# Kernel tuning notes

Measured on AMD Instinct MI355X. Metric: run time of the kernel, lower is better.

The kernel has to match this reference:

```python
import jax, jax.numpy as jnp
import numpy as np

IMAGE_SIZE = 800
OUT = 50          # feature map size
FEAT = 512
SCALES = (2.0, 4.0, 6.0)
RATIOS = (0.5, 1.0, 1.5)
A = len(SCALES) * len(RATIOS)          # 9 anchors per cell
POS_THR, NEG_THR = 0.7, 0.3
W_CONF, W_REG = 1.0, 5.0
SCALE = IMAGE_SIZE // OUT              # 16, stride of feature map


def _anchor_base():
    # order: ratio outer loop, scale inner loop (matches get_anchor_base)
    ws = jnp.array([s * r for r in RATIOS for s in SCALES], jnp.float32)  # [A]
    hs = jnp.array([s for r in RATIOS for s in SCALES], jnp.float32)      # [A]
    cx = (jnp.arange(OUT, dtype=jnp.float32) + 0.5)[:, None, None]        # grid dim0 -> x
    cy = (jnp.arange(OUT, dtype=jnp.float32) + 0.5)[None, :, None]        # grid dim1 -> y
    xmin = jnp.clip(cx - ws / 2, 0.0, OUT)
    xmax = jnp.clip(cx + ws / 2, 0.0, OUT)
    ymin = jnp.clip(cy - hs / 2, 0.0, OUT)
    ymax = jnp.clip(cy + hs / 2, 0.0, OUT)
    shp = (OUT, OUT, A)
    base = jnp.stack([jnp.broadcast_to(xmin, shp), jnp.broadcast_to(ymin, shp),
                      jnp.broadcast_to(xmax, shp), jnp.broadcast_to(ymax, shp)], axis=-1)
    return base.reshape(-1, 4)         # [N,4], N = OUT*OUT*A = 22500


def _iou(anchors, gt):
    # anchors [N,4], gt [B,M,4] (xyxy) -> iou [B,N,M]
    a = anchors[None, :, None, :]
    g = gt[:, None, :, :]
    ix1 = jnp.maximum(a[..., 0], g[..., 0]); iy1 = jnp.maximum(a[..., 1], g[..., 1])
    ix2 = jnp.minimum(a[..., 2], g[..., 2]); iy2 = jnp.minimum(a[..., 3], g[..., 3])
    inter = jnp.clip(ix2 - ix1, 0.0) * jnp.clip(iy2 - iy1, 0.0)
    area_a = (a[..., 2] - a[..., 0]) * (a[..., 3] - a[..., 1])
    area_g = (g[..., 2] - g[..., 0]) * (g[..., 3] - g[..., 1])
    return inter / (area_a + area_g - inter + 1e-8)


def _smooth_l1(d):
    ad = jnp.abs(d)
    return jnp.where(ad < 1.0, 0.5 * d * d, ad - 0.5)


def setup_inputs() -> dict:
    key = jax.random.key(0)
    ks = jax.random.split(key, 8)
    B, M = 16, 16
    features = jax.random.normal(ks[0], (B, FEAT, OUT, OUT), jnp.float32)
    # valid GT boxes in image coords: centers in [100,700], sizes in [32,200]
    cxy = jax.random.uniform(ks[1], (B, M, 2), jnp.float32, 100.0, 700.0)
    wh = jax.random.uniform(ks[2], (B, M, 2), jnp.float32, 32.0, 200.0)
    x1y1 = jnp.clip(cxy - wh / 2, 0.0, IMAGE_SIZE)
    x2y2 = jnp.clip(cxy + wh / 2, 0.0, IMAGE_SIZE)
    gt_boxes = jnp.concatenate([x1y1, x2y2], axis=-1)
    w1 = jax.random.normal(ks[3], (FEAT, FEAT, 3, 3), jnp.float32) * 0.02
    b1 = jnp.zeros((FEAT,), jnp.float32)
    w_cls = jax.random.normal(ks[4], (A, FEAT), jnp.float32) * 0.02
    b_cls = jnp.zeros((A,), jnp.float32)
    w_box = jax.random.normal(ks[5], (4 * A, FEAT), jnp.float32) * 0.02
    b_box = jnp.zeros((4 * A,), jnp.float32)
    return {"features": features, "gt_boxes": gt_boxes, "w1": w1, "b1": b1,
            "w_cls": w_cls, "b_cls": b_cls, "w_box": w_box, "b_box": b_box}


def reference(features, gt_boxes, w1, b1, w_cls, b_cls, w_box, b_box):
    B = features.shape[0]
    anchors = _anchor_base()                                   # [N,4]
    N = anchors.shape[0]

    # --- conv tower ---
    x = jax.lax.conv_general_dilated(features, w1, (1, 1), 'SAME') + b1[None, :, None, None]
    cls_map = jnp.einsum('bchw,ac->bahw', x, w_cls) + b_cls[None, :, None, None]   # [B,A,H,W]
    box_map = jnp.einsum('bchw,dc->bdhw', x, w_box) + b_box[None, :, None, None]   # [B,4A,H,W]
    logits = jnp.transpose(cls_map, (0, 2, 3, 1)).reshape(B, N)                    # [B,N]
    pred_off = jnp.transpose(box_map.reshape(B, A, 4, OUT, OUT), (0, 3, 4, 1, 2)).reshape(B, N, 4)

    # --- project gt to feature-map (anchor) coords, 'p2a' ---
    gt = gt_boxes / SCALE                                       # [B,M,4]

    # --- anchor/GT assignment ---
    iou = _iou(anchors, gt)                                     # [B,N,M]
    max_per_gt = jnp.max(iou, axis=1, keepdims=True)            # best anchor per gt
    pos_mask = ((iou == max_per_gt) & (max_per_gt > 0)) | (iou > POS_THR)  # [B,N,M]
    pos_mask = pos_mask.astype(jnp.float32)
    n_pos = jnp.maximum(pos_mask.sum(), 1.0)

    # --- gt offsets (standard tx,ty,tw,th) for every (anchor,gt) pair ---
    acx = (anchors[:, 0] + anchors[:, 2]) / 2
    acy = (anchors[:, 1] + anchors[:, 3]) / 2
    aw = jnp.maximum(anchors[:, 2] - anchors[:, 0], 1e-6)
    ah = jnp.maximum(anchors[:, 3] - anchors[:, 1], 1e-6)
    gcx = (gt[..., 0] + gt[..., 2]) / 2                         # [B,M]
    gcy = (gt[..., 1] + gt[..., 3]) / 2
    gw = jnp.maximum(gt[..., 2] - gt[..., 0], 1e-6)
    gh = jnp.maximum(gt[..., 3] - gt[..., 1], 1e-6)
    tx = (gcx[:, None, :] - acx[None, :, None]) / aw[None, :, None]   # [B,N,M]
    ty = (gcy[:, None, :] - acy[None, :, None]) / ah[None, :, None]
    tw = jnp.log(gw[:, None, :] / aw[None, :, None])
    th = jnp.log(gh[:, None, :] / ah[None, :, None])
    gt_off = jnp.stack([tx, ty, tw, th], axis=-1)               # [B,N,M,4]

    diff = gt_off - pred_off[:, :, None, :]
    reg_loss = (pos_mask[..., None] * _smooth_l1(diff)).sum() / (4.0 * n_pos)

    # --- classification loss: BCE-with-logits; positives=1, negatives=0 ---
    pos_loss = (pos_mask * jax.nn.softplus(-logits)[:, :, None]).sum() / n_pos
    neg_anchor = jnp.all(iou < NEG_THR, axis=2).astype(jnp.float32)   # [B,N]
    n_neg = jnp.maximum(neg_anchor.sum(), 1.0)
    neg_loss = (neg_anchor * jax.nn.softplus(logits)).sum() / n_neg
    cls_loss = 0.5 * (pos_loss + neg_loss)

    total_rpn_loss = W_CONF * cls_loss + W_REG * reg_loss

    # --- proposals from predicted offsets for all anchors ---
    pcx = acx[None, :] + pred_off[..., 0] * aw[None, :]
    pcy = acy[None, :] + pred_off[..., 1] * ah[None, :]
    pw = aw[None, :] * jnp.exp(pred_off[..., 2])
    ph = ah[None, :] * jnp.exp(pred_off[..., 3])
    proposals = jnp.stack([pcx - pw / 2, pcy - ph / 2, pcx + pw / 2, pcy + ph / 2], axis=-1)  # [B,N,4]

    return total_rpn_loss, proposals
```

## Files before the change

### kernel.cpp

```cpp
#include <hip/hip_runtime.h>
#include <hip/hip_bf16.h>
#include <stdint.h>


using bf16x8 = __attribute__((ext_vector_type(8))) __bf16;
using f32x4  = __attribute__((ext_vector_type(4))) float;

#define FT_CHUNK_STRIDE 2768896
#define W2_CHUNK_B 34560

__device__ __forceinline__ unsigned short f2bf(float f) {
  union { float f; unsigned u; } x; x.f = f;
  unsigned r = x.u + 0x7fffu + ((x.u >> 16) & 1u);
  return (unsigned short)(r >> 16);
}

__device__ __forceinline__ void gl_lds16(const void* g, void* l) {
  __builtin_amdgcn_global_load_lds(
      (const __attribute__((address_space(1))) void*)g,
      (__attribute__((address_space(3))) void*)l, 16, 0, 0);
}

__device__ __forceinline__ float sl1(float d) {
  float ad = fabsf(d);
  return ad < 1.f ? 0.5f * d * d : ad - 0.5f;
}
__device__ __forceinline__ float softplus_f(float x) {
  return fmaxf(x, 0.f) + log1pf(expf(-fabsf(x)));
}

__device__ __forceinline__ void anchor_strict(int n, float& ax1, float& ay1,
                                              float& ax2, float& ay2) {
  int ii = n / 450;
  int rem = n - ii * 450;
  int jj = rem / 9;
  int a  = rem - jj * 9;
  const float SC[3] = {2.f, 4.f, 6.f};
  const float RA[3] = {0.5f, 1.f, 1.5f};
  float w = __fmul_rn(SC[a % 3], RA[a / 3]);
  float h = SC[a % 3];
  float cx = __fadd_rn((float)ii, 0.5f);
  float cy = __fadd_rn((float)jj, 0.5f);
  float wh = __fmul_rn(w, 0.5f), hh = __fmul_rn(h, 0.5f);
  ax1 = fminf(fmaxf(__fsub_rn(cx, wh), 0.f), 50.f);
  ax2 = fminf(fmaxf(__fadd_rn(cx, wh), 0.f), 50.f);
  ay1 = fminf(fmaxf(__fsub_rn(cy, hh), 0.f), 50.f);
  ay2 = fminf(fmaxf(__fadd_rn(cy, hh), 0.f), 50.f);
}
__device__ __forceinline__ float iou_strict(float ax1, float ay1, float ax2, float ay2,
                                            float aarea, const float* __restrict__ g) {
  float gx1 = __fmul_rn(g[0], 0.0625f), gy1 = __fmul_rn(g[1], 0.0625f);
  float gx2 = __fmul_rn(g[2], 0.0625f), gy2 = __fmul_rn(g[3], 0.0625f);
  float ix1 = fmaxf(ax1, gx1), iy1 = fmaxf(ay1, gy1);
  float ix2 = fminf(ax2, gx2), iy2 = fminf(ay2, gy2);
  float inter = __fmul_rn(fmaxf(__fsub_rn(ix2, ix1), 0.f),
                          fmaxf(__fsub_rn(iy2, iy1), 0.f));
  float garea = __fmul_rn(__fsub_rn(gx2, gx1), __fsub_rn(gy2, gy1));
  float denom = __fadd_rn(__fsub_rn(__fadd_rn(aarea, garea), inter), 1e-8f);
  return __fdiv_rn(inter, denom);
}

__global__ __launch_bounds__(256) void k_featT(const float* __restrict__ feat,
                                               char* __restrict__ featT2) {
  const int tile = blockIdx.x;
  const int g    = blockIdx.y;
  const int b    = blockIdx.z;
  const int tid  = threadIdx.x;
  if (tile == 20) {
    uint4 z = {0, 0, 0, 0};
    for (int u = tid; u < 204 * 4; u += 256) {
      int p = u & 255; if (p >= 204) p -= 204;
      int c4 = u / 204;
      int ip, jp;
      if (p < 52)       { ip = 0;       jp = p; }
      else if (p < 104) { ip = 51;      jp = p - 52; }
      else if (p < 154) { ip = p - 103; jp = 0; }
      else              { ip = p - 153; jp = 51; }
      char* dst = featT2 + (size_t)(g * 4 + c4) * FT_CHUNK_STRIDE
                + (size_t)(b * 2704 + ip * 52 + jp) * 64;
      *(uint4*)(dst)      = z;
      *(uint4*)(dst + 16) = z;
      *(uint4*)(dst + 32) = z;
      *(uint4*)(dst + 48) = z;
    }
    return;
  }
  __shared__ __align__(16) unsigned short sT[128 * 132];
  const int pos0 = tile * 128;
  const float* fb = feat + (size_t)b * 1280000 + (size_t)(g * 128) * 2500;
  const int pq = tid & 31;
  const int rg = tid >> 5;
  const int p  = pos0 + pq * 4;
#pragma unroll
  for (int it = 0; it < 4; ++it) {
    int cb = it * 32 + rg * 4;
    float vv[4][4];
#pragma unroll
    for (int q = 0; q < 4; ++q) {
      const float* src = fb + (size_t)(cb + q) * 2500 + p;
      if (p + 3 < 2500) {
        float4 v = *(const float4*)src;
        vv[q][0] = v.x; vv[q][1] = v.y; vv[q][2] = v.z; vv[q][3] = v.w;
      } else {
#pragma unroll
        for (int e = 0; e < 4; ++e)
          vv[q][e] = fb[(size_t)(cb + q) * 2500 + min(p + e, 2499)];
      }
    }
#pragma unroll
    for (int pp = 0; pp < 4; ++pp) {
      ushort4 pk;
      pk.x = f2bf(vv[0][pp]); pk.y = f2bf(vv[1][pp]);
      pk.z = f2bf(vv[2][pp]); pk.w = f2bf(vv[3][pp]);
      *(ushort4*)&sT[(pq * 4 + pp) * 132 + cb] = pk;
    }
  }
  __syncthreads();
#pragma unroll
  for (int q2 = 0; q2 < 2; ++q2) {
    int u = tid + q2 * 256;
    int ch = u >> 7, pr = u & 127;
    int gp = pos0 + pr;
    if (gp >= 2500) continue;
    int i = gp / 50, j = gp - i * 50;
    char* dst = featT2 + (size_t)(g * 4 + ch) * FT_CHUNK_STRIDE
              + (size_t)(b * 2704 + (i + 1) * 52 + (j + 1)) * 64;
    const uint4* src = (const uint4*)&sT[pr * 132 + ch * 32];
    uint4 a0 = src[0], a1 = src[1], a2 = src[2], a3 = src[3];
    *(uint4*)(dst)      = a0;
    *(uint4*)(dst + 16) = a1;
    *(uint4*)(dst + 32) = a2;
    *(uint4*)(dst + 48) = a3;
  }
}

__global__ __launch_bounds__(128) void k_weff1(const float* __restrict__ w1,
                                               const float* __restrict__ wc,
                                               const float* __restrict__ wb,
                                               float* __restrict__ part,
                                               unsigned* __restrict__ zbuf) {
  const int t = threadIdx.x;
  if (blockIdx.x == 0 && blockIdx.y == 0) {
    for (int idx = t; idx < 264; idx += 128) zbuf[idx] = 0u;
  }
  __shared__ float sW[48][64];
  const int kmem = blockIdx.x * 128 + t;
  const int cz = blockIdx.y;
#pragma unroll
  for (int q = 0; q < 24; ++q) {
    int idx = t + q * 128;
    int co = idx >> 6, cl = idx & 63;
    int c = cz * 64 + cl;
    float v = 0.f;
    if (co < 9) v = wc[co * 512 + c];
    else if (co < 45) v = wb[(co - 9) * 512 + c];
    sW[co][cl] = v;
  }
  __syncthreads();
  float acc[48];
#pragma unroll
  for (int co = 0; co < 48; ++co) acc[co] = 0.f;
  const float* w1p = w1 + (size_t)(cz * 64) * 4608 + kmem;
  for (int c4 = 0; c4 < 64; c4 += 4) {
    float f0 = w1p[(size_t)(c4 + 0) * 4608];
    float f1 = w1p[(size_t)(c4 + 1) * 4608];
    float f2 = w1p[(size_t)(c4 + 2) * 4608];
    float f3 = w1p[(size_t)(c4 + 3) * 4608];
#pragma unroll
    for (int co = 0; co < 48; ++co) {
      float4 wv = *(const float4*)&sW[co][c4];
      acc[co] += wv.x * f0 + wv.y * f1 + wv.z * f2 + wv.w * f3;
    }
  }
  float* dst = part + (size_t)cz * 221184 + kmem;
#pragma unroll
  for (int co = 0; co < 48; ++co) dst[(size_t)co * 4608] = acc[co];
}

__global__ __launch_bounds__(256) void k_weff2(const float* __restrict__ part,
                                               unsigned short* __restrict__ w2,
                                               const float* __restrict__ wc,
                                               const float* __restrict__ wb,
                                               const float* __restrict__ b1,
                                               const float* __restrict__ bc,
                                               const float* __restrict__ bbx,
                                               float* __restrict__ bias_eff,
                                               const float* __restrict__ gt_boxes,
                                               unsigned* __restrict__ mx) {
  if (blockIdx.x >= 1128) {
    int q = blockIdx.x - 1128;
    int b = q / 88, nb = q - b * 88;
    int n = nb * 256 + threadIdx.x;
    float lm[16];
#pragma unroll
    for (int m = 0; m < 16; ++m) lm[m] = 0.f;
    if (n < 22500) {
      float ax1, ay1, ax2, ay2;
      anchor_strict(n, ax1, ay1, ax2, ay2);
      float aarea = __fmul_rn(__fsub_rn(ax2, ax1), __fsub_rn(ay2, ay1));
#pragma unroll
      for (int m = 0; m < 16; ++m)
        lm[m] = iou_strict(ax1, ay1, ax2, ay2, aarea, gt_boxes + (b * 16 + m) * 4);
    }
    __shared__ float red[4][16];
#pragma unroll
    for (int m = 0; m < 16; ++m) {
      float v = lm[m];
      for (int o = 32; o; o >>= 1) v = fmaxf(v, __shfl_down(v, o, 64));
      if ((threadIdx.x & 63) == 0) red[threadIdx.x >> 6][m] = v;
    }
    __syncthreads();
    if (threadIdx.x < 16) {
      float v = fmaxf(fmaxf(red[0][threadIdx.x], red[1][threadIdx.x]),
                      fmaxf(red[2][threadIdx.x], red[3][threadIdx.x]));
      atomicMax(mx + b * 16 + threadIdx.x, __float_as_uint(v));
    }
    return;
  }
  if (blockIdx.x >= 1080) {
    int co = blockIdx.x - 1080;
    int l = threadIdx.x;
    if (l >= 64) return;
    float s = 0.f;
#pragma unroll
    for (int q = 0; q < 8; ++q) {
      int c = q * 64 + l;
      float wv = co < 9 ? wc[co * 512 + c] : (co < 45 ? wb[(co - 9) * 512 + c] : 0.f);
      s += wv * b1[c];
    }
    for (int o = 32; o; o >>= 1) s += __shfl_down(s, o, 64);
    if (l == 0)
      bias_eff[co] = s + (co < 9 ? bc[co] : (co < 45 ? bbx[co - 9] : 0.f));
    return;
  }
  int idx = blockIdx.x * 256 + threadIdx.x;
  int c = idx / 17280;  int r = idx - c * 17280;
  int tap = r / 1920;   int r2 = r - tap * 1920;
  int co = r2 / 40;     int e = r2 - co * 40;
  float s = 0.f;
  if (e < 32) {
    int ci = c * 32 + e;
    const float* p = part + (size_t)co * 4608 + ci * 9 + tap;
#pragma unroll
    for (int cz = 0; cz < 8; ++cz) s += p[(size_t)cz * 221184];
  }
  w2[idx] = f2bf(s);
}

__global__ __launch_bounds__(256) void k_conv(const char* __restrict__ featT2,
                                              const char* __restrict__ w2,
                                              const float* __restrict__ beff,
                                              float* __restrict__ oh) {
  __shared__ __align__(16) char sF[2][19456];
  __shared__ __align__(16) char sA[2][34816];
  const int tid = threadIdx.x, lane = tid & 63, w = tid >> 6;
  const int bx = blockIdx.x;
  const int b = bx >> 4, tl = bx & 15, tr = tl >> 2, tc = tl & 3;
  const int i0 = tr * 13 - (tr == 3 ? 1 : 0);
  const int TI = (tr >= 2) ? 12 : 13;
  const int j0 = tc * 13 - (tc == 3 ? 1 : 0);
  const int TJ = (tc >= 2) ? 12 : 13;
  const int TJ2 = TJ + 2;
  const int mcount = TI * TJ;
  const int pieces = (TI + 2) * TJ2 * 5;

  const char* srcF[5];
#pragma unroll
  for (int k = 0; k < 5; ++k) {
    int s = w * 5 + k;
    int pi = s * 64 + lane;
    if (pi >= pieces) pi = pieces - 1;
    int pos = pi / 5, pc = pi - pos * 5;
    if (pc > 3) pc = 3;
    int hi = pos / TJ2, hj = pos - hi * TJ2;
    srcF[k] = featT2 + (size_t)(b * 2704 + (i0 + hi) * 52 + (j0 + hj)) * 64 + pc * 16;
  }
  int idxB[3];
#pragma unroll
  for (int bf = 0; bf < 3; ++bf) {
    int p = (w * 3 + bf) * 16 + (lane & 15);
    if (p >= mcount) p = mcount - 1;
    int di = p / TJ, dj = p - di * TJ;
    idxB[bf] = (di * TJ2 + dj) * 80 + (lane >> 4) * 16;
  }
  const int aoff = (lane & 15) * 80 + (lane >> 4) * 16;
  int toff[9];
#pragma unroll
  for (int tp = 0; tp < 9; ++tp) toff[tp] = ((tp / 3) * TJ2 + (tp % 3)) * 80;

  f32x4 acc[3][3] = {};

  auto stage = [&](int c, int pb) {
    size_t coff = (size_t)c * FT_CHUNK_STRIDE;
#pragma unroll
    for (int k = 0; k < 5; ++k) {
      int s = w * 5 + k;
      if (s < 18) gl_lds16(srcF[k] + coff, sF[pb] + s * 1024);
    }
#pragma unroll
    for (int k = 0; k < 9; ++k) {
      int s = w + 4 * k;
      if (s < 34)
        gl_lds16(w2 + (size_t)c * W2_CHUNK_B + s * 1024 + lane * 16, sA[pb] + s * 1024);
    }
  };

  stage(0, 0);
  __builtin_amdgcn_s_waitcnt(0);
  __syncthreads();

  for (int c = 0; c < 16; ++c) {
    int pb = c & 1;
    if (c < 15) stage(c + 1, pb ^ 1);
    const char* fA = sA[pb];
    const char* fB = sF[pb];
#pragma unroll
    for (int tp = 0; tp < 9; ++tp) {
      bf16x8 av[3], bv[3];
#pragma unroll
      for (int cf = 0; cf < 3; ++cf)
        av[cf] = *(const bf16x8*)(fA + tp * 3840 + cf * 1280 + aoff);
#pragma unroll
      for (int bf = 0; bf < 3; ++bf)
        bv[bf] = *(const bf16x8*)(fB + idxB[bf] + toff[tp]);
#pragma unroll
      for (int cf = 0; cf < 3; ++cf)
#pragma unroll
        for (int bf = 0; bf < 3; ++bf)
          acc[cf][bf] = __builtin_amdgcn_mfma_f32_16x16x32_bf16(av[cf], bv[bf], acc[cf][bf], 0, 0, 0);
    }
    __builtin_amdgcn_s_waitcnt(0);
    __syncthreads();
  }

  f32x4 bias[3];
#pragma unroll
  for (int cf = 0; cf < 3; ++cf)
    bias[cf] = *(const f32x4*)(beff + cf * 16 + (lane >> 4) * 4);
#pragma unroll
  for (int bf = 0; bf < 3; ++bf) {
    int p = (w * 3 + bf) * 16 + (lane & 15);
    if (p >= mcount) continue;
    int di = p / TJ, dj = p - di * TJ;
    int gm = (b * 50 + i0 + di) * 50 + (j0 + dj);
#pragma unroll
    for (int cf = 0; cf < 3; ++cf) {
      f32x4 v = acc[cf][bf];
#pragma unroll
      for (int r = 0; r < 4; ++r) v[r] += bias[cf][r];
      *(f32x4*)(oh + (size_t)gm * 48 + cf * 16 + (lane >> 4) * 4) = v;
    }
  }
}

__global__ __launch_bounds__(256) void k_loss(const float* __restrict__ gt_boxes,
                                              const unsigned* __restrict__ mxbuf,
                                              const float* __restrict__ oh,
                                              float* __restrict__ accum,
                                              float* __restrict__ dout) {
  int b = blockIdx.y;
  int n = blockIdx.x * 256 + threadIdx.x;
  float s_np = 0.f, s_reg = 0.f, s_pos = 0.f, s_nc = 0.f, s_nl = 0.f;
  if (n < 22500) {
    float ax1, ay1, ax2, ay2;
    anchor_strict(n, ax1, ay1, ax2, ay2);
    float aarea = __fmul_rn(__fsub_rn(ax2, ax1), __fsub_rn(ay2, ay1));
    float acx = (ax1 + ax2) * 0.5f, acy = (ay1 + ay2) * 0.5f;
    float aw = fmaxf(ax2 - ax1, 1e-6f), ah = fmaxf(ay2 - ay1, 1e-6f);
    int ii = n / 450, rem = n - ii * 450, jj = rem / 9, a = rem - jj * 9;
    const float* row = oh + ((size_t)(b * 2500 + ii * 50 + jj)) * 48;
    float logit = row[a];
    float p0 = row[9 + a * 4], p1 = row[10 + a * 4];
    float p2 = row[11 + a * 4], p3 = row[12 + a * 4];
    int npos = 0;
    bool allneg = true;
#pragma unroll
    for (int m = 0; m < 16; ++m) {
      const float* g = gt_boxes + (b * 16 + m) * 4;
      float iou = iou_strict(ax1, ay1, ax2, ay2, aarea, g);
      float mxv = __uint_as_float(mxbuf[b * 16 + m]);
      bool pos = ((iou == mxv) && (mxv > 0.f)) || (iou > 0.7f);
      if (iou >= 0.3f) allneg = false;
      if (pos) {
        ++npos;
        float gx1 = g[0] * 0.0625f, gy1 = g[1] * 0.0625f;
        float gx2 = g[2] * 0.0625f, gy2 = g[3] * 0.0625f;
        float gcx = (gx1 + gx2) * 0.5f, gcy = (gy1 + gy2) * 0.5f;
        float gw = fmaxf(gx2 - gx1, 1e-6f), gh = fmaxf(gy2 - gy1, 1e-6f);
        float tx = (gcx - acx) / aw, ty = (gcy - acy) / ah;
        float twv = logf(gw / aw), thv = logf(gh / ah);
        s_reg += sl1(tx - p0) + sl1(ty - p1) + sl1(twv - p2) + sl1(thv - p3);
      }
    }
    s_np = (float)npos;
    s_pos = (float)npos * softplus_f(-logit);
    if (allneg) { s_nc = 1.f; s_nl = softplus_f(logit); }
    float pcx = acx + p0 * aw, pcy = acy + p1 * ah;
    float pw = aw * expf(p2), ph = ah * expf(p3);
    float* o = dout + 1 + ((size_t)b * 22500 + n) * 4;
    o[0] = pcx - pw * 0.5f;
    o[1] = pcy - ph * 0.5f;
    o[2] = pcx + pw * 0.5f;
    o[3] = pcy + ph * 0.5f;
  }
  float vals[5] = {s_np, s_reg, s_pos, s_nc, s_nl};
  __shared__ float red[4][5];
#pragma unroll
  for (int q = 0; q < 5; ++q) {
    float v = vals[q];
    for (int o = 32; o; o >>= 1) v += __shfl_down(v, o, 64);
    if ((threadIdx.x & 63) == 0) red[threadIdx.x >> 6][q] = v;
  }
  __syncthreads();
  if (threadIdx.x < 5) {
    float v = red[0][threadIdx.x] + red[1][threadIdx.x] +
              red[2][threadIdx.x] + red[3][threadIdx.x];
    atomicAdd(accum + threadIdx.x, v);
  }
}

__global__ void k_fin(const float* __restrict__ accum, float* __restrict__ dout) {
  if (threadIdx.x == 0 && blockIdx.x == 0) {
    float np = fmaxf(accum[0], 1.f);
    float nn = fmaxf(accum[3], 1.f);
    float loss = 0.5f * (accum[2] / np + accum[4] / nn) + 5.f * (accum[1] / (4.f * np));
    dout[0] = loss;
  }
}

extern "C" void kernel_launch(void* const* d_in, const int* in_sizes, int n_in,
                              void* d_out, int out_size, void* d_ws, size_t ws_size,
                              hipStream_t stream) {
  const float* features = (const float*)d_in[0];
  const float* gt_boxes = (const float*)d_in[1];
  const float* w1    = (const float*)d_in[2];
  const float* b1    = (const float*)d_in[3];
  const float* w_cls = (const float*)d_in[4];
  const float* b_cls = (const float*)d_in[5];
  const float* w_box = (const float*)d_in[6];
  const float* b_box = (const float*)d_in[7];
  float* out = (float*)d_out;
  char* ws = (char*)d_ws;

  char*           featT2 = ws;
  unsigned short* w2     = (unsigned short*)(ws + 44302336);
  float*          wpart  = (float*)(ws + 44855296);
  float*          oh     = (float*)(ws + 51933184);
  float*          beff   = (float*)(ws + 59613184);
  unsigned*       mx     = (unsigned*)(ws + 59613376);
  float*          accum  = (float*)(ws + 59614400);

  k_featT<<<dim3(21, 4, 16), 256, 0, stream>>>(features, featT2);
  k_weff1<<<dim3(36, 8), 128, 0, stream>>>(w1, w_cls, w_box, wpart, mx);
  k_weff2<<<2536, 256, 0, stream>>>(wpart, w2, w_cls, w_box, b1, b_cls, b_box,
                                    beff, gt_boxes, mx);
  k_conv<<<256, 256, 0, stream>>>(featT2, (const char*)w2, beff, oh);
  k_loss<<<dim3(88, 16), 256, 0, stream>>>(gt_boxes, mx, oh, accum, out);
  k_fin<<<1, 64, 0, stream>>>(accum, out);
}
```

Baseline: 264.3 us.

## Fuse prep kernels, retile conv to 512 blocks, swizzle weight LDS layout

Merges the feature transpose, weight-folding and bias kernels into one launch, and moves the bias computation out of the second kernel. The weight buffer drops its padding and gains an XOR-swizzled layout to avoid LDS bank conflicts. The conv kernel now uses narrower spatial tiles (512 blocks, 2 blocks per CU) with a grid remap. The final loss reduction is folded into the loss kernel through a last-block atomic counter. Together these cut launch count, padding waste and LDS conflicts, but the counter relies on accum[5] being zeroed and adds more halo overhead per tile.

New measurement: 275.2 us. 1.04x slower.

```diff
diff --git a/kernel.cpp b/kernel.cpp
--- a/kernel.cpp
+++ b/kernel.cpp
@@ -7,7 +7,7 @@
 using f32x4  = __attribute__((ext_vector_type(4))) float;
 
 #define FT_CHUNK_STRIDE 2768896
-#define W2_CHUNK_B 34560
+#define W2_CHUNK_B 27648
 
 __device__ __forceinline__ unsigned short f2bf(float f) {
   union { float f; unsigned u; } x; x.f = f;
@@ -60,12 +60,83 @@
   return __fdiv_rn(inter, denom);
 }
 
-__global__ __launch_bounds__(256) void k_featT(const float* __restrict__ feat,
-                                               char* __restrict__ featT2) {
-  const int tile = blockIdx.x;
-  const int g    = blockIdx.y;
-  const int b    = blockIdx.z;
-  const int tid  = threadIdx.x;
+__global__ __launch_bounds__(256) void k1(const float* __restrict__ feat,
+                                          char* __restrict__ featT2,
+                                          const float* __restrict__ w1,
+                                          const float* __restrict__ wc,
+                                          const float* __restrict__ wb,
+                                          const float* __restrict__ b1,
+                                          const float* __restrict__ bc,
+                                          const float* __restrict__ bbx,
+                                          float* __restrict__ part,
+                                          float* __restrict__ bias_eff,
+                                          unsigned* __restrict__ zbuf) {
+  __shared__ __align__(16) char smem[128 * 132 * 2];
+  const int bxr = blockIdx.x;
+  const int tid = threadIdx.x;
+
+  if (bxr >= 1488) {
+    int co = bxr - 1488;
+    int l = tid;
+    if (l >= 64) return;
+    float s = 0.f;
+#pragma unroll
+    for (int q = 0; q < 8; ++q) {
+      int c = q * 64 + l;
+      float wv = co < 9 ? wc[co * 512 + c] : (co < 45 ? wb[(co - 9) * 512 + c] : 0.f);
+      s += wv * b1[c];
+    }
+    for (int o = 32; o; o >>= 1) s += __shfl_down(s, o, 64);
+    if (l == 0)
+      bias_eff[co] = s + (co < 9 ? bc[co] : (co < 45 ? bbx[co - 9] : 0.f));
+    return;
+  }
+
+  if (bxr >= 1344) {
+    int bx2 = bxr - 1344;
+    if (bx2 == 0) {
+      if (tid < 264) zbuf[tid] = 0u;
+      if (tid < 8) zbuf[256 + tid] = 0u;
+    }
+    int cz = bx2 / 18, kx = bx2 - cz * 18;
+    float* sW = (float*)smem;
+    const int kmem = kx * 256 + tid;
+#pragma unroll
+    for (int q = 0; q < 12; ++q) {
+      int idx = tid + q * 256;
+      int co = idx >> 6, cl = idx & 63;
+      int c = cz * 64 + cl;
+      float v = 0.f;
+      if (co < 9) v = wc[co * 512 + c];
+      else if (co < 45) v = wb[(co - 9) * 512 + c];
+      sW[co * 64 + cl] = v;
+    }
+    __syncthreads();
+    float acc[48];
+#pragma unroll
+    for (int co = 0; co < 48; ++co) acc[co] = 0.f;
+    const float* w1p = w1 + (size_t)(cz * 64) * 4608 + kmem;
+    for (int c4 = 0; c4 < 64; c4 += 4) {
+      float f0 = w1p[(size_t)(c4 + 0) * 4608];
+      float f1 = w1p[(size_t)(c4 + 1) * 4608];
+      float f2 = w1p[(size_t)(c4 + 2) * 4608];
+      float f3 = w1p[(size_t)(c4 + 3) * 4608];
+#pragma unroll
+      for (int co = 0; co < 48; ++co) {
+        float4 wv = *(const float4*)&sW[co * 64 + c4];
+        acc[co] += wv.x * f0 + wv.y * f1 + wv.z * f2 + wv.w * f3;
+      }
+    }
+    float* dst = part + (size_t)cz * 221184 + kmem;
+#pragma unroll
+    for (int co = 0; co < 48; ++co) dst[(size_t)co * 4608] = acc[co];
+    return;
+  }
+
+  const int tile = bxr % 21;
+  const int rest = bxr / 21;
+  const int g    = rest & 3;
+  const int b    = rest >> 2;
   if (tile == 20) {
     uint4 z = {0, 0, 0, 0};
     for (int u = tid; u < 204 * 4; u += 256) {
@@ -85,7 +156,7 @@
     }
     return;
   }
-  __shared__ __align__(16) unsigned short sT[128 * 132];
+  unsigned short* sT = (unsigned short*)smem;
   const int pos0 = tile * 128;
   const float* fb = feat + (size_t)b * 1280000 + (size_t)(g * 128) * 2500;
   const int pq = tid & 31;
@@ -134,61 +205,12 @@
   }
 }
 
-__global__ __launch_bounds__(128) void k_weff1(const float* __restrict__ w1,
-                                               const float* __restrict__ wc,
-                                               const float* __restrict__ wb,
-                                               float* __restrict__ part,
-                                               unsigned* __restrict__ zbuf) {
-  const int t = threadIdx.x;
-  if (blockIdx.x == 0 && blockIdx.y == 0) {
-    for (int idx = t; idx < 264; idx += 128) zbuf[idx] = 0u;
-  }
-  __shared__ float sW[48][64];
-  const int kmem = blockIdx.x * 128 + t;
-  const int cz = blockIdx.y;
-#pragma unroll
-  for (int q = 0; q < 24; ++q) {
-    int idx = t + q * 128;
-    int co = idx >> 6, cl = idx & 63;
-    int c = cz * 64 + cl;
-    float v = 0.f;
-    if (co < 9) v = wc[co * 512 + c];
-    else if (co < 45) v = wb[(co - 9) * 512 + c];
-    sW[co][cl] = v;
-  }
-  __syncthreads();
-  float acc[48];
-#pragma unroll
-  for (int co = 0; co < 48; ++co) acc[co] = 0.f;
-  const float* w1p = w1 + (size_t)(cz * 64) * 4608 + kmem;
-  for (int c4 = 0; c4 < 64; c4 += 4) {
-    float f0 = w1p[(size_t)(c4 + 0) * 4608];
-    float f1 = w1p[(size_t)(c4 + 1) * 4608];
-    float f2 = w1p[(size_t)(c4 + 2) * 4608];
-    float f3 = w1p[(size_t)(c4 + 3) * 4608];
-#pragma unroll
-    for (int co = 0; co < 48; ++co) {
-      float4 wv = *(const float4*)&sW[co][c4];
-      acc[co] += wv.x * f0 + wv.y * f1 + wv.z * f2 + wv.w * f3;
-    }
-  }
-  float* dst = part + (size_t)cz * 221184 + kmem;
-#pragma unroll
-  for (int co = 0; co < 48; ++co) dst[(size_t)co * 4608] = acc[co];
-}
-
-__global__ __launch_bounds__(256) void k_weff2(const float* __restrict__ part,
-                                               unsigned short* __restrict__ w2,
-                                               const float* __restrict__ wc,
-                                               const float* __restrict__ wb,
-                                               const float* __restrict__ b1,
-                                               const float* __restrict__ bc,
-                                               const float* __restrict__ bbx,
-                                               float* __restrict__ bias_eff,
-                                               const float* __restrict__ gt_boxes,
-                                               unsigned* __restrict__ mx) {
-  if (blockIdx.x >= 1128) {
-    int q = blockIdx.x - 1128;
+__global__ __launch_bounds__(256) void k2(const float* __restrict__ part,
+                                          unsigned short* __restrict__ w2,
+                                          const float* __restrict__ gt_boxes,
+                                          unsigned* __restrict__ mx) {
+  if (blockIdx.x >= 864) {
+    int q = blockIdx.x - 864;
     int b = q / 88, nb = q - b * 88;
     int n = nb * 256 + threadIdx.x;
     float lm[16];
@@ -217,57 +239,42 @@
     }
     return;
   }
-  if (blockIdx.x >= 1080) {
-    int co = blockIdx.x - 1080;
-    int l = threadIdx.x;
-    if (l >= 64) return;
-    float s = 0.f;
-#pragma unroll
-    for (int q = 0; q < 8; ++q) {
-      int c = q * 64 + l;
-      float wv = co < 9 ? wc[co * 512 + c] : (co < 45 ? wb[(co - 9) * 512 + c] : 0.f);
-      s += wv * b1[c];
-    }
-    for (int o = 32; o; o >>= 1) s += __shfl_down(s, o, 64);
-    if (l == 0)
-      bias_eff[co] = s + (co < 9 ? bc[co] : (co < 45 ? bbx[co - 9] : 0.f));
-    return;
-  }
   int idx = blockIdx.x * 256 + threadIdx.x;
-  int c = idx / 17280;  int r = idx - c * 17280;
-  int tap = r / 1920;   int r2 = r - tap * 1920;
-  int co = r2 / 40;     int e = r2 - co * 40;
+  int c = idx / 13824;  int r = idx - c * 13824;
+  int tap = r / 1536;   int r2 = r - tap * 1536;
+  int co = r2 >> 5;     int e = r2 & 31;
+  int ci = c * 32 + e;
+  const float* p = part + (size_t)co * 4608 + ci * 9 + tap;
   float s = 0.f;
-  if (e < 32) {
-    int ci = c * 32 + e;
-    const float* p = part + (size_t)co * 4608 + ci * 9 + tap;
-#pragma unroll
-    for (int cz = 0; cz < 8; ++cz) s += p[(size_t)cz * 221184];
-  }
-  w2[idx] = f2bf(s);
-}
-
-__global__ __launch_bounds__(256) void k_conv(const char* __restrict__ featT2,
-                                              const char* __restrict__ w2,
-                                              const float* __restrict__ beff,
-                                              float* __restrict__ oh) {
-  __shared__ __align__(16) char sF[2][19456];
-  __shared__ __align__(16) char sA[2][34816];
+#pragma unroll
+  for (int cz = 0; cz < 8; ++cz) s += p[(size_t)cz * 221184];
+  int boff = c * W2_CHUNK_B + tap * 3072 + (co >> 4) * 1024 + (co & 15) * 64
+           + ((((e >> 3) ^ co) & 3) << 4) + ((e & 7) << 1);
+  w2[boff >> 1] = f2bf(s);
+}
+
+__global__ __launch_bounds__(256, 2) void k3(const char* __restrict__ featT2,
+                                             const char* __restrict__ w2g,
+                                             const float* __restrict__ beff,
+                                             float* __restrict__ oh) {
+  __shared__ __align__(16) char sF[2][11264];
+  __shared__ __align__(16) char sA[2][27648];
   const int tid = threadIdx.x, lane = tid & 63, w = tid >> 6;
-  const int bx = blockIdx.x;
-  const int b = bx >> 4, tl = bx & 15, tr = tl >> 2, tc = tl & 3;
+  const int bx0 = blockIdx.x;
+  const int bx = ((bx0 & 7) << 6) | (bx0 >> 3);
+  const int b = bx >> 5, tl = bx & 31, tr = tl >> 3, tc = tl & 7;
   const int i0 = tr * 13 - (tr == 3 ? 1 : 0);
   const int TI = (tr >= 2) ? 12 : 13;
-  const int j0 = tc * 13 - (tc == 3 ? 1 : 0);
-  const int TJ = (tc >= 2) ? 12 : 13;
+  const int TJ = (tc < 2) ? 7 : 6;
+  const int j0 = (tc < 2) ? tc * 7 : 14 + (tc - 2) * 6;
   const int TJ2 = TJ + 2;
   const int mcount = TI * TJ;
   const int pieces = (TI + 2) * TJ2 * 5;
 
-  const char* srcF[5];
-#pragma unroll
-  for (int k = 0; k < 5; ++k) {
-    int s = w * 5 + k;
+  const char* srcF[3];
+#pragma unroll
+  for (int k = 0; k < 3; ++k) {
+    int s = w * 3 + k;
     int pi = s * 64 + lane;
     if (pi >= pieces) pi = pieces - 1;
     int pos = pi / 5, pc = pi - pos * 5;
@@ -275,33 +282,33 @@
     int hi = pos / TJ2, hj = pos - hi * TJ2;
     srcF[k] = featT2 + (size_t)(b * 2704 + (i0 + hi) * 52 + (j0 + hj)) * 64 + pc * 16;
   }
-  int idxB[3];
-#pragma unroll
-  for (int bf = 0; bf < 3; ++bf) {
-    int p = (w * 3 + bf) * 16 + (lane & 15);
+  int idxB[2];
+#pragma unroll
+  for (int bf = 0; bf < 2; ++bf) {
+    int p = (w * 2 + bf) * 16 + (lane & 15);
     if (p >= mcount) p = mcount - 1;
     int di = p / TJ, dj = p - di * TJ;
     idxB[bf] = (di * TJ2 + dj) * 80 + (lane >> 4) * 16;
   }
-  const int aoff = (lane & 15) * 80 + (lane >> 4) * 16;
+  const int aoff = (lane & 15) * 64 + ((((lane >> 4) ^ lane) & 3) << 4);
   int toff[9];
 #pragma unroll
   for (int tp = 0; tp < 9; ++tp) toff[tp] = ((tp / 3) * TJ2 + (tp % 3)) * 80;
 
-  f32x4 acc[3][3] = {};
+  f32x4 acc[3][2] = {};
 
   auto stage = [&](int c, int pb) {
     size_t coff = (size_t)c * FT_CHUNK_STRIDE;
 #pragma unroll
-    for (int k = 0; k < 5; ++k) {
-      int s = w * 5 + k;
-      if (s < 18) gl_lds16(srcF[k] + coff, sF[pb] + s * 1024);
-    }
-#pragma unroll
-    for (int k = 0; k < 9; ++k) {
+    for (int k = 0; k < 3; ++k) {
+      int s = w * 3 + k;
+      if (s < 11) gl_lds16(srcF[k] + coff, sF[pb] + s * 1024);
+    }
+#pragma unroll
+    for (int k = 0; k < 7; ++k) {
       int s = w + 4 * k;
-      if (s < 34)
-        gl_lds16(w2 + (size_t)c * W2_CHUNK_B + s * 1024 + lane * 16, sA[pb] + s * 1024);
+      if (s < 27)
+        gl_lds16(w2g + (size_t)c * W2_CHUNK_B + s * 1024 + lane * 16, sA[pb] + s * 1024);
     }
   };
 
@@ -316,17 +323,17 @@
     const char* fB = sF[pb];
 #pragma unroll
     for (int tp = 0; tp < 9; ++tp) {
-      bf16x8 av[3], bv[3];
+      bf16x8 av[3], bv[2];
 #pragma unroll
       for (int cf = 0; cf < 3; ++cf)
-        av[cf] = *(const bf16x8*)(fA + tp * 3840 + cf * 1280 + aoff);
-#pragma unroll
-      for (int bf = 0; bf < 3; ++bf)
+        av[cf] = *(const bf16x8*)(fA + tp * 3072 + cf * 1024 + aoff);
+#pragma unroll
+      for (int bf = 0; bf < 2; ++bf)
         bv[bf] = *(const bf16x8*)(fB + idxB[bf] + toff[tp]);
 #pragma unroll
       for (int cf = 0; cf < 3; ++cf)
 #pragma unroll
-        for (int bf = 0; bf < 3; ++bf)
+        for (int bf = 0; bf < 2; ++bf)
           acc[cf][bf] = __builtin_amdgcn_mfma_f32_16x16x32_bf16(av[cf], bv[bf], acc[cf][bf], 0, 0, 0);
     }
     __builtin_amdgcn_s_waitcnt(0);
@@ -338,8 +345,8 @@
   for (int cf = 0; cf < 3; ++cf)
     bias[cf] = *(const f32x4*)(beff + cf * 16 + (lane >> 4) * 4);
 #pragma unroll
-  for (int bf = 0; bf < 3; ++bf) {
-    int p = (w * 3 + bf) * 16 + (lane & 15);
+  for (int bf = 0; bf < 2; ++bf) {
+    int p = (w * 2 + bf) * 16 + (lane & 15);
     if (p >= mcount) continue;
     int di = p / TJ, dj = p - di * TJ;
     int gm = (b * 50 + i0 + di) * 50 + (j0 + dj);
@@ -353,11 +360,11 @@
   }
 }
 
-__global__ __launch_bounds__(256) void k_loss(const float* __restrict__ gt_boxes,
-                                              const unsigned* __restrict__ mxbuf,
-                                              const float* __restrict__ oh,
-                                              float* __restrict__ accum,
-                                              float* __restrict__ dout) {
+__global__ __launch_bounds__(256) void k4(const float* __restrict__ gt_boxes,
+                                          const unsigned* __restrict__ mxbuf,
+                                          const float* __restrict__ oh,
+                                          float* __restrict__ accum,
+                                          float* __restrict__ dout) {
   int b = blockIdx.y;
   int n = blockIdx.x * 256 + threadIdx.x;
   float s_np = 0.f, s_reg = 0.f, s_pos = 0.f, s_nc = 0.f, s_nl = 0.f;
@@ -417,14 +424,18 @@
               red[2][threadIdx.x] + red[3][threadIdx.x];
     atomicAdd(accum + threadIdx.x, v);
   }
-}
-
-__global__ void k_fin(const float* __restrict__ accum, float* __restrict__ dout) {
-  if (threadIdx.x == 0 && blockIdx.x == 0) {
-    float np = fmaxf(accum[0], 1.f);
-    float nn = fmaxf(accum[3], 1.f);
-    float loss = 0.5f * (accum[2] / np + accum[4] / nn) + 5.f * (accum[1] / (4.f * np));
-    dout[0] = loss;
+  __syncthreads();
+  if (threadIdx.x == 0) {
+    __threadfence();
+    unsigned old = atomicAdd((unsigned*)(accum + 5), 1u);
+    if (old == 1407u) {
+      float np = fmaxf(atomicAdd(accum + 0, 0.f), 1.f);
+      float rg = atomicAdd(accum + 1, 0.f);
+      float pp = atomicAdd(accum + 2, 0.f);
+      float nn = fmaxf(atomicAdd(accum + 3, 0.f), 1.f);
+      float nl = atomicAdd(accum + 4, 0.f);
+      dout[0] = 0.5f * (pp / np + nl / nn) + 5.f * (rg / (4.f * np));
+    }
   }
 }
 
@@ -450,11 +461,9 @@
   unsigned*       mx     = (unsigned*)(ws + 59613376);
   float*          accum  = (float*)(ws + 59614400);
 
-  k_featT<<<dim3(21, 4, 16), 256, 0, stream>>>(features, featT2);
-  k_weff1<<<dim3(36, 8), 128, 0, stream>>>(w1, w_cls, w_box, wpart, mx);
-  k_weff2<<<2536, 256, 0, stream>>>(wpart, w2, w_cls, w_box, b1, b_cls, b_box,
-                                    beff, gt_boxes, mx);
-  k_conv<<<256, 256, 0, stream>>>(featT2, (const char*)w2, beff, oh);
-  k_loss<<<dim3(88, 16), 256, 0, stream>>>(gt_boxes, mx, oh, accum, out);
-  k_fin<<<1, 64, 0, stream>>>(accum, out);
-}
+  k1<<<1536, 256, 0, stream>>>(features, featT2, w1, w_cls, w_box, b1, b_cls,
+                               b_box, wpart, beff, mx);
+  k2<<<2272, 256, 0, stream>>>(wpart, w2, gt_boxes, mx);
+  k3<<<512, 256, 0, stream>>>(featT2, (const char*)w2, beff, oh);
+  k4<<<dim3(88, 16), 256, 0, stream>>>(gt_boxes, mx, oh, accum, out);
+}
```
